# Optimization experiments

Hardware: AMD Instinct MI355X
Metric: run time of the kernel (lower is better)

The kernel has to match this reference:

```python
import jax, jax.numpy as jnp
import numpy as np

B, IN_DIM, HID = 32768, 512, 1024
# fixed triangle graph buffer from the module
SRC = jnp.array([0, 1, 2, 1, 2, 0], dtype=jnp.int32)
TGT = jnp.array([1, 2, 0, 0, 1, 2], dtype=jnp.int32)


def setup_inputs() -> dict:
    key = jax.random.key(0)
    ks = jax.random.split(key, 16)
    s_in = 1.0 / np.sqrt(IN_DIM)
    s_h = 1.0 / np.sqrt(HID)
    return {
        "x": jax.random.normal(ks[0], (B, IN_DIM), jnp.float32),
        # encoder: Linear(IN,HID) -> ReLU -> Linear(HID,HID) -> ReLU
        "enc_w1": jax.random.uniform(ks[1], (IN_DIM, HID), jnp.float32, -s_in, s_in),
        "enc_b1": jax.random.uniform(ks[2], (HID,), jnp.float32, -s_in, s_in),
        "enc_w2": jax.random.uniform(ks[3], (HID, HID), jnp.float32, -s_h, s_h),
        "enc_b2": jax.random.uniform(ks[4], (HID,), jnp.float32, -s_h, s_h),
        "init_nodes": jax.random.normal(ks[5], (3, HID), jnp.float32),
        # GIN layer 1 MLP: Linear -> ReLU -> Linear
        "gin1_w1": jax.random.uniform(ks[6], (HID, HID), jnp.float32, -s_h, s_h),
        "gin1_b1": jax.random.uniform(ks[7], (HID,), jnp.float32, -s_h, s_h),
        "gin1_w2": jax.random.uniform(ks[8], (HID, HID), jnp.float32, -s_h, s_h),
        "gin1_b2": jax.random.uniform(ks[9], (HID,), jnp.float32, -s_h, s_h),
        # GIN layer 2 MLP
        "gin2_w1": jax.random.uniform(ks[10], (HID, HID), jnp.float32, -s_h, s_h),
        "gin2_b1": jax.random.uniform(ks[11], (HID,), jnp.float32, -s_h, s_h),
        "gin2_w2": jax.random.uniform(ks[12], (HID, HID), jnp.float32, -s_h, s_h),
        "gin2_b2": jax.random.uniform(ks[13], (HID,), jnp.float32, -s_h, s_h),
        # decoder: Linear(HID, 1)
        "dec_w": jax.random.uniform(ks[14], (HID, 1), jnp.float32, -s_h, s_h),
        "dec_b": jax.random.uniform(ks[15], (1,), jnp.float32, -s_h, s_h),
    }


def _gin_conv(h, w1, b1, w2, b2):
    # h: [B, 3, H]; sum-aggregate neighbor features along fixed edge list, eps=0
    agg = jnp.zeros_like(h).at[:, TGT, :].add(h[:, SRC, :])
    m = h + agg  # (1+eps)*x + aggregate, eps=0
    m = jax.nn.relu(jnp.einsum('bnh,hk->bnk', m, w1) + b1)
    return jnp.einsum('bnh,hk->bnk', m, w2) + b2


def reference(x, enc_w1, enc_b1, enc_w2, enc_b2, init_nodes,
              gin1_w1, gin1_b1, gin1_w2, gin1_b2,
              gin2_w1, gin2_b1, gin2_w2, gin2_b2,
              dec_w, dec_b):
    # encoder (vectorized over batch)
    e = jax.nn.relu(x @ enc_w1 + enc_b1)
    e = jax.nn.relu(e @ enc_w2 + enc_b2)  # [B, H]
    # per-sample node init, batched: [B, 3, H]
    h = init_nodes[None, :, :] + e[:, None, :]
    h = jax.nn.relu(_gin_conv(h, gin1_w1, gin1_b1, gin1_w2, gin1_b2))
    h = jax.nn.relu(_gin_conv(h, gin2_w1, gin2_b1, gin2_w2, gin2_b2))
    out = (jnp.einsum('bnh,ho->bno', h, dec_w) + dec_b)[..., 0]  # [B, 3]
    return out
```

## Files before the change

### kernel.cpp

```cpp
#include <hip/hip_runtime.h>
#include <stdint.h>

#define AS1 __attribute__((address_space(1)))
#define AS3 __attribute__((address_space(3)))

typedef unsigned short ushort_t;
typedef __attribute__((ext_vector_type(8))) short bf16x8;
typedef __attribute__((ext_vector_type(4))) float f32x4;

__device__ __forceinline__ ushort_t f2bf(float f) {
  union { float f; uint32_t u; } c; c.f = f;
  uint32_t u = c.u;
  return (ushort_t)((u + 0x7fffu + ((u >> 16) & 1u)) >> 16);
}


__global__ __launch_bounds__(256) void k_cvt4(const float* __restrict__ in,
                                              ushort_t* __restrict__ out, int n4) {
  int i = blockIdx.x * blockDim.x + threadIdx.x;
  int stride = gridDim.x * blockDim.x;
  for (; i < n4; i += stride) {
    float4 v = ((const float4*)in)[i];
    ushort4 o;
    o.x = f2bf(v.x); o.y = f2bf(v.y); o.z = f2bf(v.z); o.w = f2bf(v.w);
    ((ushort4*)out)[i] = o;
  }
}

__global__ __launch_bounds__(256) void k_suminit(const float* __restrict__ init,
                                                 float* __restrict__ s) {
  int i = blockIdx.x * 256 + threadIdx.x;
  if (i < 1024) s[i] = init[i] + init[i + 1024] + init[i + 2048];
}

__global__ __launch_bounds__(256) void k_transpose(const float* __restrict__ W,
                                                   ushort_t* __restrict__ Wt,
                                                   int K, int N) {
  __shared__ float tile[32][33];
  int tx = threadIdx.x & 31, ty = threadIdx.x >> 5;
  int n0 = blockIdx.x * 32, k0 = blockIdx.y * 32;
  #pragma unroll
  for (int i = ty; i < 32; i += 8)
    tile[i][tx] = W[(size_t)(k0 + i) * N + (n0 + tx)];
  __syncthreads();
  #pragma unroll
  for (int i = ty; i < 32; i += 8)
    Wt[(size_t)(n0 + i) * K + (k0 + tx)] = f2bf(tile[tx][i]);
}


template <int KT, int EPI>
__global__ __launch_bounds__(256, 2)
void gemm_bt(const ushort_t* __restrict__ A, const ushort_t* __restrict__ Bt,
             const float* __restrict__ bias, const float* __restrict__ extra,
             ushort_t* __restrict__ C, float* __restrict__ part) {
  __shared__ char smem[65536];

  const int nwg = gridDim.x;
  const int cpx = nwg >> 3;
  int bid = blockIdx.x;
  int wg = (bid & 7) * cpx + (bid >> 3);
  const int mt = wg >> 3;
  const int nt = wg & 7;

  const int t = threadIdx.x;
  const int wave = t >> 6;
  const int lane = t & 63;
  const int wr = wave >> 1, wc = wave & 1;
  const int lrow = lane & 15;
  const int kq = lane >> 4;

  const char* Abase = (const char*)A + (size_t)mt * 128 * (KT * 2);
  const char* Bbase = (const char*)Bt + (size_t)nt * 128 * (KT * 2);

  const int rbase = wave * 8 + (lane >> 3);
  const int colOff = ((lane & 7) ^ (rbase & 7)) << 4;

  f32x4 acc[4][4];
  #pragma unroll
  for (int m = 0; m < 4; ++m)
    #pragma unroll
    for (int n = 0; n < 4; ++n)
      acc[m][n] = (f32x4){0.f, 0.f, 0.f, 0.f};

  constexpr int NKT = KT / 64;

  {
    char* sA = smem;
    char* sB = smem + 16384;
    #pragma unroll
    for (int i = 0; i < 4; ++i) {
      int r = i * 32 + rbase;
      __builtin_amdgcn_global_load_lds(
          (const AS1 void*)(Abase + (size_t)r * (KT * 2) + colOff),
          (AS3 void*)(sA + i * 4096 + wave * 1024), 16, 0, 0);
      __builtin_amdgcn_global_load_lds(
          (const AS1 void*)(Bbase + (size_t)r * (KT * 2) + colOff),
          (AS3 void*)(sB + i * 4096 + wave * 1024), 16, 0, 0);
    }
  }

  int cur = 0;
  for (int kt = 0; kt < NKT; ++kt) {
    if (kt + 1 < NKT) {
      const size_t kb = (size_t)(kt + 1) * 128;
      char* sA = smem + (cur ^ 1) * 32768;
      char* sB = sA + 16384;
      #pragma unroll
      for (int i = 0; i < 4; ++i) {
        int r = i * 32 + rbase;
        __builtin_amdgcn_global_load_lds(
            (const AS1 void*)(Abase + (size_t)r * (KT * 2) + kb + colOff),
            (AS3 void*)(sA + i * 4096 + wave * 1024), 16, 0, 0);
        __builtin_amdgcn_global_load_lds(
            (const AS1 void*)(Bbase + (size_t)r * (KT * 2) + kb + colOff),
            (AS3 void*)(sB + i * 4096 + wave * 1024), 16, 0, 0);
      }
      asm volatile("s_waitcnt vmcnt(8)" ::: "memory");
    } else {
      asm volatile("s_waitcnt vmcnt(0)" ::: "memory");
    }
    __builtin_amdgcn_s_barrier();
    asm volatile("" ::: "memory");

    const char* smA = smem + cur * 32768;
    const char* smB = smA + 16384;
    #pragma unroll
    for (int ks = 0; ks < 2; ++ks) {
      bf16x8 af[4], bfv[4];
      #pragma unroll
      for (int m = 0; m < 4; ++m) {
        int r = wr * 64 + m * 16 + lrow;
        af[m] = *(const bf16x8*)(smA + r * 128 +
                                 ((ks * 64 + kq * 16) ^ ((r & 7) << 4)));
      }
      #pragma unroll
      for (int n = 0; n < 4; ++n) {
        int r = wc * 64 + n * 16 + lrow;
        bfv[n] = *(const bf16x8*)(smB + r * 128 +
                                  ((ks * 64 + kq * 16) ^ ((r & 7) << 4)));
      }
      #pragma unroll
      for (int m = 0; m < 4; ++m)
        #pragma unroll
        for (int n = 0; n < 4; ++n)
          acc[m][n] = __builtin_amdgcn_mfma_f32_16x16x32_bf16(af[m], bfv[n],
                                                              acc[m][n], 0, 0, 0);
    }
    asm volatile("" ::: "memory");
    __builtin_amdgcn_s_barrier();
    asm volatile("" ::: "memory");
    cur ^= 1;
  }

  const int row0 = mt * 128 + wr * 64;
  const int col0 = nt * 128 + wc * 64;
  if (EPI == 3) {
    float s[4][4];
    #pragma unroll
    for (int m = 0; m < 4; ++m)
      #pragma unroll
      for (int j = 0; j < 4; ++j) s[m][j] = 0.f;
    #pragma unroll
    for (int n = 0; n < 4; ++n) {
      int col = col0 + n * 16 + lrow;
      float bn = bias[col];
      float wn = extra[col];
      #pragma unroll
      for (int m = 0; m < 4; ++m)
        #pragma unroll
        for (int j = 0; j < 4; ++j) {
          float v = fmaxf(acc[m][n][j] + bn, 0.f);
          s[m][j] += v * wn;
        }
    }
    const int slot = nt * 2 + wc;
    #pragma unroll
    for (int m = 0; m < 4; ++m)
      #pragma unroll
      for (int j = 0; j < 4; ++j) {
        float v = s[m][j];
        v += __shfl_xor(v, 1);
        v += __shfl_xor(v, 2);
        v += __shfl_xor(v, 4);
        v += __shfl_xor(v, 8);
        if (lrow == 0)
          part[(size_t)slot * 32768 + (row0 + m * 16 + kq * 4 + j)] = v;
      }
  } else {
    #pragma unroll
    for (int n = 0; n < 4; ++n) {
      int col = col0 + n * 16 + lrow;
      float bn = bias[col];
      float en = 0.f;
      if (EPI == 1) en = extra[col];
      #pragma unroll
      for (int m = 0; m < 4; ++m) {
        int rb = row0 + m * 16 + kq * 4;
        #pragma unroll
        for (int j = 0; j < 4; ++j) {
          float v = acc[m][n][j] + bn;
          v = fmaxf(v, 0.f);
          if (EPI == 1) v = 3.f * v + en;
          else if (EPI == 2) v = 3.f * v;
          C[(size_t)(rb + j) * 1024 + col] = f2bf(v);
        }
      }
    }
  }
}


__global__ __launch_bounds__(256) void k_decfinal(const float* __restrict__ part,
                                                  const float* __restrict__ db,
                                                  float* __restrict__ out) {
  int r = blockIdx.x * 256 + threadIdx.x;
  float s = 0.f;
  #pragma unroll
  for (int i = 0; i < 16; ++i) s += part[(size_t)i * 32768 + r];
  float v = s + db[0];
  out[r * 3 + 0] = v;
  out[r * 3 + 1] = v;
  out[r * 3 + 2] = v;
}


extern "C" void kernel_launch(void* const* d_in, const int* in_sizes, int n_in,
                              void* d_out, int out_size, void* d_ws, size_t ws_size,
                              hipStream_t stream) {
  const float* x      = (const float*)d_in[0];
  const float* enc_w1 = (const float*)d_in[1];
  const float* enc_b1 = (const float*)d_in[2];
  const float* enc_w2 = (const float*)d_in[3];
  const float* enc_b2 = (const float*)d_in[4];
  const float* initn  = (const float*)d_in[5];
  const float* g1w1   = (const float*)d_in[6];
  const float* g1b1   = (const float*)d_in[7];
  const float* g1w2   = (const float*)d_in[8];
  const float* g1b2   = (const float*)d_in[9];
  const float* g2w1   = (const float*)d_in[10];
  const float* g2b1   = (const float*)d_in[11];
  const float* g2w2   = (const float*)d_in[12];
  const float* g2b2   = (const float*)d_in[13];
  const float* dec_w  = (const float*)d_in[14];
  const float* dec_b  = (const float*)d_in[15];
  float* out = (float*)d_out;

  char* ws = (char*)d_ws;
  ushort_t* xb    = (ushort_t*)(ws + 0);
  ushort_t* wtE1  = (ushort_t*)(ws + 33554432);
  ushort_t* wtE2  = (ushort_t*)(ws + 34603008);
  ushort_t* wtG11 = (ushort_t*)(ws + 36700160);
  ushort_t* wtG12 = (ushort_t*)(ws + 38797312);
  ushort_t* wtG21 = (ushort_t*)(ws + 40894464);
  ushort_t* wtG22 = (ushort_t*)(ws + 42991616);
  float*    sInit = (float*)   (ws + 45088768);
  ushort_t* bufA  = (ushort_t*)(ws + 45092864);
  ushort_t* bufB  = (ushort_t*)(ws + 112201728);
  float*    part  = (float*)   (ws + 112201728);

  k_cvt4<<<2048, 256, 0, stream>>>(x, xb, 32768 * 512 / 4);
  k_suminit<<<4, 256, 0, stream>>>(initn, sInit);
  {
    dim3 g512(32, 16), g1024(32, 32);
    k_transpose<<<g512, 256, 0, stream>>>(enc_w1, wtE1, 512, 1024);
    k_transpose<<<g1024, 256, 0, stream>>>(enc_w2, wtE2, 1024, 1024);
    k_transpose<<<g1024, 256, 0, stream>>>(g1w1, wtG11, 1024, 1024);
    k_transpose<<<g1024, 256, 0, stream>>>(g1w2, wtG12, 1024, 1024);
    k_transpose<<<g1024, 256, 0, stream>>>(g2w1, wtG21, 1024, 1024);
    k_transpose<<<g1024, 256, 0, stream>>>(g2w2, wtG22, 1024, 1024);
  }

  gemm_bt<512, 0><<<2048, 256, 0, stream>>>(xb, wtE1, enc_b1, nullptr, bufA, nullptr);
  gemm_bt<1024, 1><<<2048, 256, 0, stream>>>(bufA, wtE2, enc_b2, sInit, bufB, nullptr);
  gemm_bt<1024, 0><<<2048, 256, 0, stream>>>(bufB, wtG11, g1b1, nullptr, bufA, nullptr);
  gemm_bt<1024, 2><<<2048, 256, 0, stream>>>(bufA, wtG12, g1b2, nullptr, bufB, nullptr);
  gemm_bt<1024, 0><<<2048, 256, 0, stream>>>(bufB, wtG21, g2b1, nullptr, bufA, nullptr);
  gemm_bt<1024, 3><<<2048, 256, 0, stream>>>(bufA, wtG22, g2b2, dec_w, nullptr, part);
  k_decfinal<<<128, 256, 0, stream>>>(part, dec_b, out);
}
```

Measured before the change: 404.7 us.

## Use 256x256 tiles with an 8-wave phased MFMA/load schedule in GEMM

Grows the bf16 GEMM block tile from 128x128 to 256x256 and uses 512 threads (8 waves), each wave computing a 128x64 sub-tile. The K loop becomes a phased schedule: two 64-wide K tiles live in 128KB of LDS, and global-to-LDS loads of half-tiles are interleaved with four MFMA phases bracketed by barriers and s_setprio. The aim is to raise arithmetic intensity per byte loaded and keep matrix cores busy while copies are in flight. In exchange, the large LDS footprint limits occupancy to one block per CU, and the many barriers add synchronisation cost; the grid shrinks to 512 blocks.

```diff
diff --git a/kernel.cpp b/kernel.cpp
--- a/kernel.cpp
+++ b/kernel.cpp
@@ -49,134 +49,173 @@
 }
 
 
+#define LDA(sbase, mh) do { \
+  _Pragma("unroll") for (int mq_ = 0; mq_ < 4; ++mq_) { \
+    const int r_ = wmB + (mh) * 64 + mq_ * 16 + lrow; \
+    const char* rp_ = (sbase) + r_ * 128; \
+    const int sw_ = (r_ & 7) << 4; \
+    a[mq_][0] = *(const bf16x8*)(rp_ + ((kq16) ^ sw_)); \
+    a[mq_][1] = *(const bf16x8*)(rp_ + ((64 + kq16) ^ sw_)); \
+  } } while (0)
+
+#define LDB(sbase, nh) do { \
+  _Pragma("unroll") for (int nq_ = 0; nq_ < 2; ++nq_) { \
+    const int r_ = wnB + (nh) * 32 + nq_ * 16 + lrow; \
+    const char* rp_ = (sbase) + r_ * 128; \
+    const int sw_ = (r_ & 7) << 4; \
+    b[nh][nq_][0] = *(const bf16x8*)(rp_ + ((kq16) ^ sw_)); \
+    b[nh][nq_][1] = *(const bf16x8*)(rp_ + ((64 + kq16) ^ sw_)); \
+  } } while (0)
+
+#define MM(mh, nh) do { \
+  _Pragma("unroll") for (int mq_ = 0; mq_ < 4; ++mq_) \
+  _Pragma("unroll") for (int nq_ = 0; nq_ < 2; ++nq_) { \
+    acc[(mh) * 4 + mq_][(nh) * 2 + nq_] = __builtin_amdgcn_mfma_f32_16x16x32_bf16( \
+        a[mq_][0], b[nh][nq_][0], acc[(mh) * 4 + mq_][(nh) * 2 + nq_], 0, 0, 0); \
+    acc[(mh) * 4 + mq_][(nh) * 2 + nq_] = __builtin_amdgcn_mfma_f32_16x16x32_bf16( \
+        a[mq_][1], b[nh][nq_][1], acc[(mh) * 4 + mq_][(nh) * 2 + nq_], 0, 0, 0); \
+  } } while (0)
+
+#define STAGE_A(sbase, tile, half) do { \
+  const size_t kb_ = (size_t)(tile) * 128; \
+  _Pragma("unroll") for (int l_ = 0; l_ < 2; ++l_) { \
+    const int row_ = l_ * 128 + (half) * 64 + r5; \
+    __builtin_amdgcn_global_load_lds( \
+        (const AS1 void*)(Ag + (size_t)row_ * KTB + kb_ + colOff), \
+        (AS3 void*)((sbase) + (l_ * 128 + (half) * 64 + w8) * 128), 16, 0, 0); \
+  } } while (0)
+
+#define STAGE_B(sbase, tile, half) do { \
+  const size_t kb_ = (size_t)(tile) * 128; \
+  _Pragma("unroll") for (int l_ = 0; l_ < 2; ++l_) { \
+    const int row_ = l_ * 128 + (half) * 32 + bRowT; \
+    __builtin_amdgcn_global_load_lds( \
+        (const AS1 void*)(Bg + (size_t)row_ * KTB + kb_ + colOff), \
+        (AS3 void*)((sbase) + (l_ * 128 + (half) * 32 + bRowW) * 128), 16, 0, 0); \
+  } } while (0)
+
+#define PH_OPEN do { asm volatile("" ::: "memory"); __builtin_amdgcn_s_barrier(); \
+                     __builtin_amdgcn_s_setprio(1); } while (0)
+#define PH_CLOSE do { __builtin_amdgcn_s_setprio(0); asm volatile("" ::: "memory"); \
+                      __builtin_amdgcn_s_barrier(); } while (0)
+#define PH_CLOSE_W(N) do { __builtin_amdgcn_s_setprio(0); \
+                      asm volatile("s_waitcnt vmcnt(" #N ")" ::: "memory"); \
+                      __builtin_amdgcn_s_barrier(); } while (0)
+
 template <int KT, int EPI>
-__global__ __launch_bounds__(256, 2)
+__global__ __launch_bounds__(512, 2)
 void gemm_bt(const ushort_t* __restrict__ A, const ushort_t* __restrict__ Bt,
              const float* __restrict__ bias, const float* __restrict__ extra,
              ushort_t* __restrict__ C, float* __restrict__ part) {
-  __shared__ char smem[65536];
-
-  const int nwg = gridDim.x;
-  const int cpx = nwg >> 3;
-  int bid = blockIdx.x;
-  int wg = (bid & 7) * cpx + (bid >> 3);
-  const int mt = wg >> 3;
-  const int nt = wg & 7;
+  constexpr int KTB = KT * 2;
+  constexpr int NKT = KT / 64;
+  constexpr int NI = NKT / 2;
+
+  __shared__ char smem[131072];
+  char* ldsA0 = smem;
+  char* ldsB0 = smem + 32768;
+  char* ldsA1 = smem + 65536;
+  char* ldsB1 = smem + 98304;
+
+  const int cpx = gridDim.x >> 3;
+  const int bid = blockIdx.x;
+  const int wg = (bid & 7) * cpx + (bid >> 3);
+  const int mt = wg >> 2;
+  const int nt = wg & 3;
 
   const int t = threadIdx.x;
-  const int wave = t >> 6;
+  const int w = t >> 6;
   const int lane = t & 63;
-  const int wr = wave >> 1, wc = wave & 1;
+  const int wm = w >> 2;
+  const int wn = w & 3;
   const int lrow = lane & 15;
   const int kq = lane >> 4;
-
-  const char* Abase = (const char*)A + (size_t)mt * 128 * (KT * 2);
-  const char* Bbase = (const char*)Bt + (size_t)nt * 128 * (KT * 2);
-
-  const int rbase = wave * 8 + (lane >> 3);
-  const int colOff = ((lane & 7) ^ (rbase & 7)) << 4;
-
-  f32x4 acc[4][4];
+  const int kq16 = kq << 4;
+  const int wmB = wm * 128;
+  const int wnB = wn * 64;
+
+  const int r5 = t >> 3;
+  const int colOff = ((t & 7) ^ (r5 & 7)) << 4;
+  const int w8 = w << 3;
+  const int bRowT = (r5 & 31) + ((r5 >> 5) << 6);
+  const int bRowW = ((w >> 2) << 6) + ((w & 3) << 3);
+
+  const char* Ag = (const char*)A + (size_t)mt * 256 * KTB;
+  const char* Bg = (const char*)Bt + (size_t)nt * 256 * KTB;
+
+  f32x4 acc[8][4];
   #pragma unroll
-  for (int m = 0; m < 4; ++m)
+  for (int m = 0; m < 8; ++m)
     #pragma unroll
     for (int n = 0; n < 4; ++n)
       acc[m][n] = (f32x4){0.f, 0.f, 0.f, 0.f};
 
-  constexpr int NKT = KT / 64;
-
-  {
-    char* sA = smem;
-    char* sB = smem + 16384;
-    #pragma unroll
-    for (int i = 0; i < 4; ++i) {
-      int r = i * 32 + rbase;
-      __builtin_amdgcn_global_load_lds(
-          (const AS1 void*)(Abase + (size_t)r * (KT * 2) + colOff),
-          (AS3 void*)(sA + i * 4096 + wave * 1024), 16, 0, 0);
-      __builtin_amdgcn_global_load_lds(
-          (const AS1 void*)(Bbase + (size_t)r * (KT * 2) + colOff),
-          (AS3 void*)(sB + i * 4096 + wave * 1024), 16, 0, 0);
-    }
+  bf16x8 a[4][2];
+  bf16x8 b[2][2][2];
+
+  STAGE_A(ldsA0, 0, 0);
+  STAGE_B(ldsB0, 0, 1);
+  STAGE_A(ldsA0, 0, 1);
+  STAGE_B(ldsB0, 0, 0);
+  STAGE_A(ldsA1, 1, 0);
+  STAGE_B(ldsB1, 1, 1);
+  asm volatile("s_waitcnt vmcnt(4)" ::: "memory");
+  __builtin_amdgcn_s_barrier();
+
+  #pragma unroll 1
+  for (int it = 0; it < NI; ++it) {
+    const int t1 = 2 * it + 1, t2 = 2 * it + 2, t3 = 2 * it + 3;
+    const bool more = (it + 1 < NI);
+    LDA(ldsA0, 0);
+    LDB(ldsB0, 0);
+    STAGE_A(ldsA1, t1, 1);
+    PH_OPEN; MM(0, 0); PH_CLOSE;
+    LDB(ldsB0, 1);
+    STAGE_B(ldsB1, t1, 0);
+    PH_OPEN; MM(0, 1); PH_CLOSE;
+    LDA(ldsA0, 1);
+    if (more) STAGE_A(ldsA0, t2, 0);
+    PH_OPEN; MM(1, 1); PH_CLOSE;
+    if (more) STAGE_B(ldsB0, t2, 1);
+    PH_OPEN; MM(1, 0);
+    if (more) { PH_CLOSE_W(4); } else { PH_CLOSE_W(0); }
+    LDA(ldsA1, 0);
+    LDB(ldsB1, 0);
+    if (more) STAGE_A(ldsA0, t2, 1);
+    PH_OPEN; MM(0, 0); PH_CLOSE;
+    LDB(ldsB1, 1);
+    if (more) STAGE_B(ldsB0, t2, 0);
+    PH_OPEN; MM(0, 1); PH_CLOSE;
+    LDA(ldsA1, 1);
+    if (more) STAGE_A(ldsA1, t3, 0);
+    PH_OPEN; MM(1, 1); PH_CLOSE;
+    if (more) STAGE_B(ldsB1, t3, 1);
+    PH_OPEN; MM(1, 0);
+    if (more) { PH_CLOSE_W(4); } else { PH_CLOSE_W(0); }
   }
 
-  int cur = 0;
-  for (int kt = 0; kt < NKT; ++kt) {
-    if (kt + 1 < NKT) {
-      const size_t kb = (size_t)(kt + 1) * 128;
-      char* sA = smem + (cur ^ 1) * 32768;
-      char* sB = sA + 16384;
-      #pragma unroll
-      for (int i = 0; i < 4; ++i) {
-        int r = i * 32 + rbase;
-        __builtin_amdgcn_global_load_lds(
-            (const AS1 void*)(Abase + (size_t)r * (KT * 2) + kb + colOff),
-            (AS3 void*)(sA + i * 4096 + wave * 1024), 16, 0, 0);
-        __builtin_amdgcn_global_load_lds(
-            (const AS1 void*)(Bbase + (size_t)r * (KT * 2) + kb + colOff),
-            (AS3 void*)(sB + i * 4096 + wave * 1024), 16, 0, 0);
-      }
-      asm volatile("s_waitcnt vmcnt(8)" ::: "memory");
-    } else {
-      asm volatile("s_waitcnt vmcnt(0)" ::: "memory");
-    }
-    __builtin_amdgcn_s_barrier();
-    asm volatile("" ::: "memory");
-
-    const char* smA = smem + cur * 32768;
-    const char* smB = smA + 16384;
-    #pragma unroll
-    for (int ks = 0; ks < 2; ++ks) {
-      bf16x8 af[4], bfv[4];
-      #pragma unroll
-      for (int m = 0; m < 4; ++m) {
-        int r = wr * 64 + m * 16 + lrow;
-        af[m] = *(const bf16x8*)(smA + r * 128 +
-                                 ((ks * 64 + kq * 16) ^ ((r & 7) << 4)));
-      }
-      #pragma unroll
-      for (int n = 0; n < 4; ++n) {
-        int r = wc * 64 + n * 16 + lrow;
-        bfv[n] = *(const bf16x8*)(smB + r * 128 +
-                                  ((ks * 64 + kq * 16) ^ ((r & 7) << 4)));
-      }
-      #pragma unroll
-      for (int m = 0; m < 4; ++m)
-        #pragma unroll
-        for (int n = 0; n < 4; ++n)
-          acc[m][n] = __builtin_amdgcn_mfma_f32_16x16x32_bf16(af[m], bfv[n],
-                                                              acc[m][n], 0, 0, 0);
-    }
-    asm volatile("" ::: "memory");
-    __builtin_amdgcn_s_barrier();
-    asm volatile("" ::: "memory");
-    cur ^= 1;
-  }
-
-  const int row0 = mt * 128 + wr * 64;
-  const int col0 = nt * 128 + wc * 64;
+  const int row0 = mt * 256 + wm * 128;
+  const int col0 = nt * 256 + wn * 64;
   if (EPI == 3) {
-    float s[4][4];
-    #pragma unroll
-    for (int m = 0; m < 4; ++m)
+    float s[8][4];
+    #pragma unroll
+    for (int m = 0; m < 8; ++m)
       #pragma unroll
       for (int j = 0; j < 4; ++j) s[m][j] = 0.f;
     #pragma unroll
     for (int n = 0; n < 4; ++n) {
       int col = col0 + n * 16 + lrow;
       float bn = bias[col];
-      float wn = extra[col];
+      float wnv = extra[col];
       #pragma unroll
-      for (int m = 0; m < 4; ++m)
+      for (int m = 0; m < 8; ++m)
         #pragma unroll
-        for (int j = 0; j < 4; ++j) {
-          float v = fmaxf(acc[m][n][j] + bn, 0.f);
-          s[m][j] += v * wn;
-        }
+        for (int j = 0; j < 4; ++j)
+          s[m][j] += fmaxf(acc[m][n][j] + bn, 0.f) * wnv;
     }
-    const int slot = nt * 2 + wc;
-    #pragma unroll
-    for (int m = 0; m < 4; ++m)
+    const int slot = nt * 4 + wn;
+    #pragma unroll
+    for (int m = 0; m < 8; ++m)
       #pragma unroll
       for (int j = 0; j < 4; ++j) {
         float v = s[m][j];
@@ -195,7 +234,7 @@
       float en = 0.f;
       if (EPI == 1) en = extra[col];
       #pragma unroll
-      for (int m = 0; m < 4; ++m) {
+      for (int m = 0; m < 8; ++m) {
         int rb = row0 + m * 16 + kq * 4;
         #pragma unroll
         for (int j = 0; j < 4; ++j) {
@@ -271,11 +310,11 @@
     k_transpose<<<g1024, 256, 0, stream>>>(g2w2, wtG22, 1024, 1024);
   }
 
-  gemm_bt<512, 0><<<2048, 256, 0, stream>>>(xb, wtE1, enc_b1, nullptr, bufA, nullptr);
-  gemm_bt<1024, 1><<<2048, 256, 0, stream>>>(bufA, wtE2, enc_b2, sInit, bufB, nullptr);
-  gemm_bt<1024, 0><<<2048, 256, 0, stream>>>(bufB, wtG11, g1b1, nullptr, bufA, nullptr);
-  gemm_bt<1024, 2><<<2048, 256, 0, stream>>>(bufA, wtG12, g1b2, nullptr, bufB, nullptr);
-  gemm_bt<1024, 0><<<2048, 256, 0, stream>>>(bufB, wtG21, g2b1, nullptr, bufA, nullptr);
-  gemm_bt<1024, 3><<<2048, 256, 0, stream>>>(bufA, wtG22, g2b2, dec_w, nullptr, part);
+  gemm_bt<512, 0><<<512, 512, 0, stream>>>(xb, wtE1, enc_b1, nullptr, bufA, nullptr);
+  gemm_bt<1024, 1><<<512, 512, 0, stream>>>(bufA, wtE2, enc_b2, sInit, bufB, nullptr);
+  gemm_bt<1024, 0><<<512, 512, 0, stream>>>(bufB, wtG11, g1b1, nullptr, bufA, nullptr);
+  gemm_bt<1024, 2><<<512, 512, 0, stream>>>(bufA, wtG12, g1b2, nullptr, bufB, nullptr);
+  gemm_bt<1024, 0><<<512, 512, 0, stream>>>(bufB, wtG21, g2b1, nullptr, bufA, nullptr);
+  gemm_bt<1024, 3><<<512, 512, 0, stream>>>(bufA, wtG22, g2b2, dec_w, nullptr, part);
   k_decfinal<<<128, 256, 0, stream>>>(part, dec_b, out);
 }
```

Result: slower. 434.1 us (+7.3%).

## Drop LDS double buffering in GEMM to halve shared memory, reorder epilogue stores

Applied to the files above, without the earlier changes.

Replaces the double-buffered LDS prefetch pipeline with a single 32KB buffer that is loaded, synchronized, consumed and synchronized again on each K step. This halves LDS use per workgroup, which may let more workgroups share a CU, but it removes the overlap of global loads with MFMA compute. The epilogue also hoists the bias and extra loads and reorders the store loops so that each output row is written as one group of four columns.

```diff
diff --git a/kernel.cpp b/kernel.cpp
--- a/kernel.cpp
+++ b/kernel.cpp
@@ -54,7 +54,9 @@
 void gemm_bt(const ushort_t* __restrict__ A, const ushort_t* __restrict__ Bt,
              const float* __restrict__ bias, const float* __restrict__ extra,
              ushort_t* __restrict__ C, float* __restrict__ part) {
-  __shared__ char smem[65536];
+  __shared__ char smem[32768];
+  char* smA = smem;
+  char* smB = smem + 16384;
 
   const int nwg = gridDim.x;
   const int cpx = nwg >> 3;
@@ -84,47 +86,19 @@
       acc[m][n] = (f32x4){0.f, 0.f, 0.f, 0.f};
 
   constexpr int NKT = KT / 64;
-
-  {
-    char* sA = smem;
-    char* sB = smem + 16384;
+  for (int kt = 0; kt < NKT; ++kt) {
+    const size_t kb = (size_t)kt * 128;
     #pragma unroll
     for (int i = 0; i < 4; ++i) {
       int r = i * 32 + rbase;
       __builtin_amdgcn_global_load_lds(
-          (const AS1 void*)(Abase + (size_t)r * (KT * 2) + colOff),
-          (AS3 void*)(sA + i * 4096 + wave * 1024), 16, 0, 0);
+          (const AS1 void*)(Abase + (size_t)r * (KT * 2) + kb + colOff),
+          (AS3 void*)(smA + i * 4096 + wave * 1024), 16, 0, 0);
       __builtin_amdgcn_global_load_lds(
-          (const AS1 void*)(Bbase + (size_t)r * (KT * 2) + colOff),
-          (AS3 void*)(sB + i * 4096 + wave * 1024), 16, 0, 0);
-    }
-  }
-
-  int cur = 0;
-  for (int kt = 0; kt < NKT; ++kt) {
-    if (kt + 1 < NKT) {
-      const size_t kb = (size_t)(kt + 1) * 128;
-      char* sA = smem + (cur ^ 1) * 32768;
-      char* sB = sA + 16384;
-      #pragma unroll
-      for (int i = 0; i < 4; ++i) {
-        int r = i * 32 + rbase;
-        __builtin_amdgcn_global_load_lds(
-            (const AS1 void*)(Abase + (size_t)r * (KT * 2) + kb + colOff),
-            (AS3 void*)(sA + i * 4096 + wave * 1024), 16, 0, 0);
-        __builtin_amdgcn_global_load_lds(
-            (const AS1 void*)(Bbase + (size_t)r * (KT * 2) + kb + colOff),
-            (AS3 void*)(sB + i * 4096 + wave * 1024), 16, 0, 0);
-      }
-      asm volatile("s_waitcnt vmcnt(8)" ::: "memory");
-    } else {
-      asm volatile("s_waitcnt vmcnt(0)" ::: "memory");
-    }
-    __builtin_amdgcn_s_barrier();
-    asm volatile("" ::: "memory");
-
-    const char* smA = smem + cur * 32768;
-    const char* smB = smA + 16384;
+          (const AS1 void*)(Bbase + (size_t)r * (KT * 2) + kb + colOff),
+          (AS3 void*)(smB + i * 4096 + wave * 1024), 16, 0, 0);
+    }
+    __syncthreads();
     #pragma unroll
     for (int ks = 0; ks < 2; ++ks) {
       bf16x8 af[4], bfv[4];
@@ -147,10 +121,7 @@
           acc[m][n] = __builtin_amdgcn_mfma_f32_16x16x32_bf16(af[m], bfv[n],
                                                               acc[m][n], 0, 0, 0);
     }
-    asm volatile("" ::: "memory");
-    __builtin_amdgcn_s_barrier();
-    asm volatile("" ::: "memory");
-    cur ^= 1;
+    __syncthreads();
   }
 
   const int row0 = mt * 128 + wr * 64;
@@ -188,22 +159,26 @@
           part[(size_t)slot * 32768 + (row0 + m * 16 + kq * 4 + j)] = v;
       }
   } else {
+    float bn[4], en[4];
     #pragma unroll
     for (int n = 0; n < 4; ++n) {
       int col = col0 + n * 16 + lrow;
-      float bn = bias[col];
-      float en = 0.f;
-      if (EPI == 1) en = extra[col];
-      #pragma unroll
-      for (int m = 0; m < 4; ++m) {
-        int rb = row0 + m * 16 + kq * 4;
+      bn[n] = bias[col];
+      en[n] = (EPI == 1) ? extra[col] : 0.f;
+    }
+    #pragma unroll
+    for (int m = 0; m < 4; ++m) {
+      #pragma unroll
+      for (int j = 0; j < 4; ++j) {
+        int rb = row0 + m * 16 + kq * 4 + j;
+        ushort_t* Crow = C + (size_t)rb * 1024 + col0 + lrow;
         #pragma unroll
-        for (int j = 0; j < 4; ++j) {
-          float v = acc[m][n][j] + bn;
+        for (int n = 0; n < 4; ++n) {
+          float v = acc[m][n][j] + bn[n];
           v = fmaxf(v, 0.f);
-          if (EPI == 1) v = 3.f * v + en;
+          if (EPI == 1) v = 3.f * v + en[n];
           else if (EPI == 2) v = 3.f * v;
-          C[(size_t)(rb + j) * 1024 + col] = f2bf(v);
+          Crow[n * 16] = f2bf(v);
         }
       }
     }
```

Result: faster. 379.4 us (-6.2%).
